# Kernel optimization log

Measured on AMD Instinct MI355X. Metric: run time of the kernel, lower is better.

The kernel has to match this reference:

```python
import jax, jax.numpy as jnp
import numpy as np

N_NODES = 100000
N_EDGES = 1600000
N_GRAPHS = 512
IN_DIM = 128
HID = 128
N_CLASSES = 10


def _gcn_conv(x, W, b, src, dst, n):
    """PyG GCNConv: out = D^{-1/2} (A+I) D^{-1/2} (x @ W) + b."""
    xw = x @ W  # [n, out_dim]
    loop = jnp.arange(n)
    s = jnp.concatenate([src, loop])  # add self loops
    d = jnp.concatenate([dst, loop])
    deg = jax.ops.segment_sum(jnp.ones(s.shape, dtype=xw.dtype), d, num_segments=n)
    dinv = jnp.where(deg > 0, jax.lax.rsqrt(deg), jnp.zeros((), xw.dtype))
    norm = dinv[s] * dinv[d]  # [E + n]
    out = jax.ops.segment_sum(xw[s] * norm[:, None], d, num_segments=n)
    return out + b


def _global_mean_pool(x, batch, num_graphs):
    sums = jax.ops.segment_sum(x, batch, num_segments=num_graphs)
    cnts = jax.ops.segment_sum(jnp.ones(batch.shape, dtype=x.dtype), batch, num_segments=num_graphs)
    return sums / jnp.maximum(cnts, 1.0)[:, None]


def setup_inputs() -> dict:
    key = jax.random.key(0)
    ks = jax.random.split(key, 8)
    x = jax.random.normal(ks[0], (N_NODES, IN_DIM), dtype=jnp.float32)
    edge_index = jax.random.randint(ks[1], (2, N_EDGES), 0, N_NODES, dtype=jnp.int64)
    batch = jnp.sort(jax.random.randint(ks[2], (N_NODES,), 0, N_GRAPHS, dtype=jnp.int64))
    sc = 1.0 / np.sqrt(IN_DIM)
    W1 = jax.random.normal(ks[3], (IN_DIM, HID), dtype=jnp.float32) * sc
    b1 = jnp.zeros((HID,), dtype=jnp.float32)
    W2 = jax.random.normal(ks[4], (HID, HID), dtype=jnp.float32) * (1.0 / np.sqrt(HID))
    b2 = jnp.zeros((HID,), dtype=jnp.float32)
    Wc = jax.random.normal(ks[5], (HID, N_CLASSES), dtype=jnp.float32) * (1.0 / np.sqrt(HID))
    bc = jnp.zeros((N_CLASSES,), dtype=jnp.float32)
    return {"x": x, "edge_index": edge_index, "batch": batch,
            "W1": W1, "b1": b1, "W2": W2, "b2": b2, "Wc": Wc, "bc": bc}


def reference(x, edge_index, batch, W1, b1, W2, b2, Wc, bc):
    src, dst = edge_index[0], edge_index[1]
    n = x.shape[0]
    h = _gcn_conv(x, W1, b1, src, dst, n)
    h = jax.nn.relu(h)
    h = _gcn_conv(h, W2, b2, src, dst, n)
    g = _global_mean_pool(h, batch, N_GRAPHS)
    return g @ Wc + bc
```

## Files before the change

### kernel.cpp

```cpp
#include <hip/hip_runtime.h>

#define N_NODES 100000
#define N_EDGES 1600000
#define N_GRAPHS 512
#define DIM 128
#define NCLS 10
#define NBKT 782
#define BCAP 2560

typedef __attribute__((ext_vector_type(8))) short short8;
typedef __attribute__((ext_vector_type(4))) float f32x4;

static __device__ __forceinline__ unsigned short f2bf(float f) {
    unsigned u = __float_as_uint(f);
    unsigned r = (u + 0x7FFF + ((u >> 16) & 1)) >> 16;
    return (unsigned short)r;
}
static __device__ __forceinline__ float bf2f(unsigned u) {
    return __uint_as_float(u << 16);
}


__global__ void k_zero(int* __restrict__ bcnt) {
    int i = blockIdx.x * 256 + threadIdx.x;
    if (i < NBKT) bcnt[i] = 0;
}

__global__ __launch_bounds__(256) void k_bucket(
    const int* __restrict__ src, const int* __restrict__ dst,
    int* __restrict__ bcnt, unsigned* __restrict__ bpack, int E) {
    __shared__ int cnt[NBKT];
    __shared__ int base[NBKT];
    int tid = threadIdx.x;
    for (int i = tid; i < NBKT; i += 256) cnt[i] = 0;
    __syncthreads();
    int e0 = blockIdx.x * 4096 + tid;
    unsigned pk[16]; short bk[16];
#pragma unroll
    for (int j = 0; j < 16; j++) {
        int e = e0 + j * 256;
        if (e < E) {
            int s = src[e], d = dst[e];
            bk[j] = (short)(d >> 7);
            pk[j] = ((unsigned)(d & 127) << 17) | (unsigned)s;
            atomicAdd(&cnt[bk[j]], 1);
        } else bk[j] = -1;
    }
    __syncthreads();
    for (int i = tid; i < NBKT; i += 256) {
        int c = cnt[i];
        base[i] = c ? atomicAdd(&bcnt[i], c) : 0;
        cnt[i] = 0;
    }
    __syncthreads();
#pragma unroll
    for (int j = 0; j < 16; j++) {
        if (bk[j] >= 0) {
            int p = base[bk[j]] + atomicAdd(&cnt[bk[j]], 1);
            if (p < BCAP) bpack[(size_t)bk[j] * BCAP + p] = pk[j];
        }
    }
}

__global__ __launch_bounds__(256) void k_bscan(const int* __restrict__ bcnt,
                                               int* __restrict__ bbase) {
    __shared__ int lds[256];
    int tid = threadIdx.x;
    int v[4], pre[4];
    int s = 0;
#pragma unroll
    for (int j = 0; j < 4; j++) {
        int idx = tid * 4 + j;
        v[j] = (idx < NBKT) ? min(bcnt[idx], BCAP) : 0;
        pre[j] = s; s += v[j];
    }
    lds[tid] = s;
    __syncthreads();
    for (int off = 1; off < 256; off <<= 1) {
        int t = (tid >= off) ? lds[tid - off] : 0;
        __syncthreads();
        lds[tid] += t;
        __syncthreads();
    }
    int excl = lds[tid] - s;
#pragma unroll
    for (int j = 0; j < 4; j++) {
        int idx = tid * 4 + j;
        if (idx < NBKT) bbase[idx] = excl + pre[j];
    }
}

__global__ __launch_bounds__(256) void k_bsort(
    const unsigned* __restrict__ bpack, const int* __restrict__ bcnt,
    const int* __restrict__ bbase, int* __restrict__ rp, float* __restrict__ dinv,
    int* __restrict__ esrc, int N) {
    __shared__ int cnt[128];
    __shared__ int scan[128];
    __shared__ int cur[128];
    int b = blockIdx.x, tid = threadIdx.x;
    int n0 = b << 7;
    int m = min(bcnt[b], BCAP);
    int gbase = bbase[b];
    const unsigned* bp = bpack + (size_t)b * BCAP;
    if (tid < 128) cnt[tid] = 0;
    __syncthreads();
    for (int j = tid; j < m; j += 256) atomicAdd(&cnt[bp[j] >> 17], 1);
    __syncthreads();
    if (tid < 128) scan[tid] = cnt[tid];
    __syncthreads();
    for (int off = 1; off < 128; off <<= 1) {
        int t = (tid < 128 && tid >= off) ? scan[tid - off] : 0;
        __syncthreads();
        if (tid < 128) scan[tid] += t;
        __syncthreads();
    }
    if (tid < 128) {
        int c = cnt[tid];
        int excl = scan[tid] - c;
        int node = n0 + tid;
        if (node <= N) rp[node] = gbase + excl;
        if (node < N) dinv[node] = rsqrtf((float)(c + 1));
        cur[tid] = gbase + excl;
    }
    __syncthreads();
    for (int j = tid; j < m; j += 256) {
        unsigned pk = bp[j];
        int p = atomicAdd(&cur[pk >> 17], 1);
        esrc[p] = (int)(pk & 0x1FFFF);
    }
}


__global__ void k_wprep(const float* __restrict__ W, unsigned short* __restrict__ wfrag) {
    int t = blockIdx.x * 256 + threadIdx.x;
    int j = t & 7, lane = (t >> 3) & 63, nt = (t >> 9) & 7, kit = t >> 12;
    int k = kit * 32 + (lane >> 4) * 8 + j;
    int n = nt * 16 + (lane & 15);
    float v = W[k * 128 + n];
    unsigned short h = f2bf(v);
    wfrag[t] = h;
    wfrag[16384 + t] = f2bf(v - bf2f(h));
}


__global__ __launch_bounds__(256) void k_gemm_f32(
    const float* __restrict__ A, const unsigned short* __restrict__ wfrag,
    const float* __restrict__ dinv, unsigned short* __restrict__ ybf, int M) {
    __shared__ unsigned short scr[4 * 32 * 136];
    int tid = threadIdx.x, wave = tid >> 6, lane = tid & 63;
    int m = lane & 15, quad = lane >> 4;
    int rowBase = blockIdx.x * 128 + wave * 32;
    int r0 = rowBase + m, r1 = rowBase + 16 + m;
    f32x4 acc0[8], acc1[8];
#pragma unroll
    for (int i = 0; i < 8; i++) { acc0[i] = (f32x4){0,0,0,0}; acc1[i] = (f32x4){0,0,0,0}; }
    const unsigned short* whi = wfrag;
    const unsigned short* wlo = wfrag + 16384;

#pragma unroll
    for (int kit = 0; kit < 4; kit++) {
        float a0[8], a1[8];
        if (r0 < M) {
            const float4* ap = (const float4*)(A + (size_t)r0 * 128 + kit * 32 + quad * 8);
            float4 f0 = ap[0], f1 = ap[1];
            a0[0]=f0.x; a0[1]=f0.y; a0[2]=f0.z; a0[3]=f0.w; a0[4]=f1.x; a0[5]=f1.y; a0[6]=f1.z; a0[7]=f1.w;
        } else { for (int j = 0; j < 8; j++) a0[j] = 0.f; }
        if (r1 < M) {
            const float4* ap = (const float4*)(A + (size_t)r1 * 128 + kit * 32 + quad * 8);
            float4 f0 = ap[0], f1 = ap[1];
            a1[0]=f0.x; a1[1]=f0.y; a1[2]=f0.z; a1[3]=f0.w; a1[4]=f1.x; a1[5]=f1.y; a1[6]=f1.z; a1[7]=f1.w;
        } else { for (int j = 0; j < 8; j++) a1[j] = 0.f; }
        short8 ahi0, alo0, ahi1, alo1;
#pragma unroll
        for (int j = 0; j < 8; j++) {
            unsigned short h0 = f2bf(a0[j]);
            ahi0[j] = (short)h0; alo0[j] = (short)f2bf(a0[j] - bf2f(h0));
            unsigned short h1 = f2bf(a1[j]);
            ahi1[j] = (short)h1; alo1[j] = (short)f2bf(a1[j] - bf2f(h1));
        }
        int fb = kit * 4096 + lane * 8;
#pragma unroll
        for (int nt = 0; nt < 8; nt++) {
            int idx = fb + nt * 512;
            short8 bhi = *(const short8*)(whi + idx);
            short8 blo = *(const short8*)(wlo + idx);
            acc0[nt] = __builtin_amdgcn_mfma_f32_16x16x32_bf16(ahi0, bhi, acc0[nt], 0, 0, 0);
            acc0[nt] = __builtin_amdgcn_mfma_f32_16x16x32_bf16(alo0, bhi, acc0[nt], 0, 0, 0);
            acc0[nt] = __builtin_amdgcn_mfma_f32_16x16x32_bf16(ahi0, blo, acc0[nt], 0, 0, 0);
            acc1[nt] = __builtin_amdgcn_mfma_f32_16x16x32_bf16(ahi1, bhi, acc1[nt], 0, 0, 0);
            acc1[nt] = __builtin_amdgcn_mfma_f32_16x16x32_bf16(alo1, bhi, acc1[nt], 0, 0, 0);
            acc1[nt] = __builtin_amdgcn_mfma_f32_16x16x32_bf16(ahi1, blo, acc1[nt], 0, 0, 0);
        }
    }
    float dv0 = (r0 < M) ? dinv[r0] : 0.f;
    float dv1 = (r1 < M) ? dinv[r1] : 0.f;
    unsigned short* wsm = scr + wave * 32 * 136;
#pragma unroll
    for (int rg = 0; rg < 4; rg++) {
        float s0 = __shfl(dv0, quad * 4 + rg);
        float s1 = __shfl(dv1, quad * 4 + rg);
#pragma unroll
        for (int nt = 0; nt < 8; nt++) {
            wsm[(quad * 4 + rg) * 136 + nt * 16 + m] = f2bf(acc0[nt][rg] * s0);
            wsm[(16 + quad * 4 + rg) * 136 + nt * 16 + m] = f2bf(acc1[nt][rg] * s1);
        }
    }
    __syncthreads();
#pragma unroll
    for (int i = 0; i < 8; i++) {
        int rl = i * 4 + quad;
        int grow = rowBase + rl;
        if (grow < M) {
            short8 v = *(const short8*)(wsm + rl * 136 + m * 8);
            *(short8*)(ybf + (size_t)grow * 128 + m * 8) = v;
        }
    }
}


__global__ __launch_bounds__(256) void k_gemm_bf(
    const unsigned short* __restrict__ A, const unsigned short* __restrict__ wfrag,
    const float* __restrict__ dinv, unsigned short* __restrict__ ybf, int M) {
    __shared__ unsigned short scr[4 * 32 * 136];
    int tid = threadIdx.x, wave = tid >> 6, lane = tid & 63;
    int m = lane & 15, quad = lane >> 4;
    int rowBase = blockIdx.x * 128 + wave * 32;
    int r0 = rowBase + m, r1 = rowBase + 16 + m;
    f32x4 acc0[8], acc1[8];
#pragma unroll
    for (int i = 0; i < 8; i++) { acc0[i] = (f32x4){0,0,0,0}; acc1[i] = (f32x4){0,0,0,0}; }
    const unsigned short* whi = wfrag;
    const unsigned short* wlo = wfrag + 16384;

#pragma unroll
    for (int kit = 0; kit < 4; kit++) {
        short8 ah0, ah1;
        if (r0 < M) ah0 = *(const short8*)(A + (size_t)r0 * 128 + kit * 32 + quad * 8);
        else { for (int j = 0; j < 8; j++) ah0[j] = 0; }
        if (r1 < M) ah1 = *(const short8*)(A + (size_t)r1 * 128 + kit * 32 + quad * 8);
        else { for (int j = 0; j < 8; j++) ah1[j] = 0; }
        int fb = kit * 4096 + lane * 8;
#pragma unroll
        for (int nt = 0; nt < 8; nt++) {
            int idx = fb + nt * 512;
            short8 bhi = *(const short8*)(whi + idx);
            short8 blo = *(const short8*)(wlo + idx);
            acc0[nt] = __builtin_amdgcn_mfma_f32_16x16x32_bf16(ah0, bhi, acc0[nt], 0, 0, 0);
            acc0[nt] = __builtin_amdgcn_mfma_f32_16x16x32_bf16(ah0, blo, acc0[nt], 0, 0, 0);
            acc1[nt] = __builtin_amdgcn_mfma_f32_16x16x32_bf16(ah1, bhi, acc1[nt], 0, 0, 0);
            acc1[nt] = __builtin_amdgcn_mfma_f32_16x16x32_bf16(ah1, blo, acc1[nt], 0, 0, 0);
        }
    }
    float dv0 = (r0 < M) ? dinv[r0] : 0.f;
    float dv1 = (r1 < M) ? dinv[r1] : 0.f;
    unsigned short* wsm = scr + wave * 32 * 136;
#pragma unroll
    for (int rg = 0; rg < 4; rg++) {
        float s0 = __shfl(dv0, quad * 4 + rg);
        float s1 = __shfl(dv1, quad * 4 + rg);
#pragma unroll
        for (int nt = 0; nt < 8; nt++) {
            wsm[(quad * 4 + rg) * 136 + nt * 16 + m] = f2bf(acc0[nt][rg] * s0);
            wsm[(16 + quad * 4 + rg) * 136 + nt * 16 + m] = f2bf(acc1[nt][rg] * s1);
        }
    }
    __syncthreads();
#pragma unroll
    for (int i = 0; i < 8; i++) {
        int rl = i * 4 + quad;
        int grow = rowBase + rl;
        if (grow < M) {
            short8 v = *(const short8*)(wsm + rl * 136 + m * 8);
            *(short8*)(ybf + (size_t)grow * 128 + m * 8) = v;
        }
    }
}


__global__ __launch_bounds__(256) void k_agg(
    const unsigned short* __restrict__ y, const float* __restrict__ dinv,
    const int* __restrict__ rp, const int* __restrict__ esrc,
    const float* __restrict__ bias, unsigned* __restrict__ out, int relu, int N) {
    int wave = threadIdx.x >> 6;
    int lane = threadIdx.x & 63;
    int node = blockIdx.x * 4 + wave;
    if (node >= N) return;
    const unsigned* y2 = (const unsigned*)y;
    unsigned vs = y2[(size_t)node * 64 + lane];
    float a0 = bf2f(vs & 0xFFFF), a1 = bf2f(vs >> 16);
    int beg = rp[node], end = rp[node + 1];
    int j = beg;
    for (; j + 8 <= end; j += 8) {
        int s0 = esrc[j], s1 = esrc[j + 1], s2 = esrc[j + 2], s3 = esrc[j + 3];
        int s4 = esrc[j + 4], s5 = esrc[j + 5], s6 = esrc[j + 6], s7 = esrc[j + 7];
        unsigned v0 = y2[(size_t)s0 * 64 + lane];
        unsigned v1 = y2[(size_t)s1 * 64 + lane];
        unsigned v2 = y2[(size_t)s2 * 64 + lane];
        unsigned v3 = y2[(size_t)s3 * 64 + lane];
        unsigned v4 = y2[(size_t)s4 * 64 + lane];
        unsigned v5 = y2[(size_t)s5 * 64 + lane];
        unsigned v6 = y2[(size_t)s6 * 64 + lane];
        unsigned v7 = y2[(size_t)s7 * 64 + lane];
        a0 += bf2f(v0 & 0xFFFF); a1 += bf2f(v0 >> 16);
        a0 += bf2f(v1 & 0xFFFF); a1 += bf2f(v1 >> 16);
        a0 += bf2f(v2 & 0xFFFF); a1 += bf2f(v2 >> 16);
        a0 += bf2f(v3 & 0xFFFF); a1 += bf2f(v3 >> 16);
        a0 += bf2f(v4 & 0xFFFF); a1 += bf2f(v4 >> 16);
        a0 += bf2f(v5 & 0xFFFF); a1 += bf2f(v5 >> 16);
        a0 += bf2f(v6 & 0xFFFF); a1 += bf2f(v6 >> 16);
        a0 += bf2f(v7 & 0xFFFF); a1 += bf2f(v7 >> 16);
    }
    for (; j < end; j++) {
        unsigned v = y2[(size_t)esrc[j] * 64 + lane];
        a0 += bf2f(v & 0xFFFF); a1 += bf2f(v >> 16);
    }
    float s = dinv[node];
    float2 bv = ((const float2*)bias)[lane];
    float o0 = s * a0 + bv.x;
    float o1 = s * a1 + bv.y;
    if (relu) { o0 = fmaxf(o0, 0.f); o1 = fmaxf(o1, 0.f); }
    out[(size_t)node * 64 + lane] = (unsigned)f2bf(o0) | ((unsigned)f2bf(o1) << 16);
}


__global__ __launch_bounds__(256) void k_pool(
    const unsigned* __restrict__ h2, const int* __restrict__ batch,
    float* __restrict__ g, int n) {
    __shared__ float2 red[4][64];
    int gid = blockIdx.x;
    int tid = threadIdx.x, wave = tid >> 6, lane = tid & 63;
    int lo = 0, hi = n;
    while (lo < hi) { int mid = (lo + hi) >> 1; if (batch[mid] < gid) lo = mid + 1; else hi = mid; }
    int start = lo;
    hi = n;
    while (lo < hi) { int mid = (lo + hi) >> 1; if (batch[mid] < gid + 1) lo = mid + 1; else hi = mid; }
    int end = lo;
    float a0 = 0.f, a1 = 0.f;
    for (int r = start + wave; r < end; r += 4) {
        unsigned v = h2[(size_t)r * 64 + lane];
        a0 += bf2f(v & 0xFFFF); a1 += bf2f(v >> 16);
    }
    red[wave][lane] = make_float2(a0, a1);
    __syncthreads();
    if (tid < 64) {
        float2 s = red[0][tid];
        s.x += red[1][tid].x; s.y += red[1][tid].y;
        s.x += red[2][tid].x; s.y += red[2][tid].y;
        s.x += red[3][tid].x; s.y += red[3][tid].y;
        int cnt = end - start;
        float inv = 1.f / (float)(cnt > 0 ? cnt : 1);
        ((float2*)g)[gid * 64 + tid] = make_float2(s.x * inv, s.y * inv);
    }
}


__global__ __launch_bounds__(128) void k_final(
    const float* __restrict__ g, const float* __restrict__ Wc,
    const float* __restrict__ bc, float* __restrict__ out) {
    __shared__ float row[DIM];
    int gid = blockIdx.x;
    row[threadIdx.x] = g[gid * DIM + threadIdx.x];
    __syncthreads();
    int c = threadIdx.x;
    if (c < NCLS) {
        float acc = bc[c];
#pragma unroll 16
        for (int k = 0; k < DIM; k++) acc += row[k] * Wc[k * NCLS + c];
        out[gid * NCLS + c] = acc;
    }
}

extern "C" void kernel_launch(void* const* d_in, const int* in_sizes, int n_in,
                              void* d_out, int out_size, void* d_ws, size_t ws_size,
                              hipStream_t stream) {
    const float* x    = (const float*)d_in[0];
    const int*   ei   = (const int*)d_in[1];
    const int*   batch= (const int*)d_in[2];
    const float* W1   = (const float*)d_in[3];
    const float* b1   = (const float*)d_in[4];
    const float* W2   = (const float*)d_in[5];
    const float* b2   = (const float*)d_in[6];
    const float* Wc   = (const float*)d_in[7];
    const float* bc   = (const float*)d_in[8];
    float* out = (float*)d_out;
    const int N = N_NODES, E = N_EDGES;
    const int* src = ei;
    const int* dst = ei + E;

    char* ws = (char*)d_ws;
    size_t off = 0;
    auto carve = [&](size_t bytes) -> void* {
        void* p = ws + off;
        off = (off + bytes + 255) & ~(size_t)255;
        return p;
    };
    int*      rp    = (int*)     carve((size_t)(N + 1) * 4);
    float*    dinv  = (float*)   carve((size_t)N * 4);
    int*      bcnt  = (int*)     carve(NBKT * 4);
    int*      bbase = (int*)     carve(NBKT * 4);
    unsigned* bpack = (unsigned*)carve((size_t)NBKT * BCAP * 4);
    int*      esrc  = (int*)     carve((size_t)E * 4);
    unsigned short* wf1 = (unsigned short*)carve(2 * 16384 * 2);
    unsigned short* wf2 = (unsigned short*)carve(2 * 16384 * 2);
    unsigned short* bufY = (unsigned short*)carve((size_t)N * DIM * 2);
    unsigned short* bufH = (unsigned short*)carve((size_t)N * DIM * 2);
    float*    g     = (float*)   carve((size_t)N_GRAPHS * DIM * 4);
    (void)ws_size; (void)n_in; (void)in_sizes; (void)out_size;

    hipLaunchKernelGGL(k_zero,   dim3((NBKT + 255) / 256), dim3(256), 0, stream, bcnt);
    hipLaunchKernelGGL(k_wprep,  dim3(64), dim3(256), 0, stream, W1, wf1);
    hipLaunchKernelGGL(k_wprep,  dim3(64), dim3(256), 0, stream, W2, wf2);
    hipLaunchKernelGGL(k_bucket, dim3((E + 4095) / 4096), dim3(256), 0, stream, src, dst, bcnt, bpack, E);
    hipLaunchKernelGGL(k_bscan,  dim3(1), dim3(256), 0, stream, bcnt, bbase);
    hipLaunchKernelGGL(k_bsort,  dim3(NBKT), dim3(256), 0, stream, bpack, bcnt, bbase, rp, dinv, esrc, N);

    int gemmGrid = (N + 127) / 128;
    hipLaunchKernelGGL(k_gemm_f32, dim3(gemmGrid), dim3(256), 0, stream, x, wf1, dinv, bufY, N);
    hipLaunchKernelGGL(k_agg, dim3((N + 3) / 4), dim3(256), 0, stream, bufY, dinv, rp, esrc, b1, (unsigned*)bufH, 1, N);
    hipLaunchKernelGGL(k_gemm_bf, dim3(gemmGrid), dim3(256), 0, stream, bufH, wf2, dinv, bufY, N);
    hipLaunchKernelGGL(k_agg, dim3((N + 3) / 4), dim3(256), 0, stream, bufY, dinv, rp, esrc, b2, (unsigned*)bufH, 0, N);
    hipLaunchKernelGGL(k_pool,  dim3(N_GRAPHS), dim3(256), 0, stream, (const unsigned*)bufH, batch, g, N);
    hipLaunchKernelGGL(k_final, dim3(N_GRAPHS), dim3(128), 0, stream, g, Wc, bc, out);
}
```

Measured before the change: 377.3 us.

## Store node features in four column-chunk planes for cache-friendly aggregation

The node-feature buffers are split into four planes of 32 bf16 columns each ([4][N][32]). The GEMM epilogues write this layout, the second GEMM reads its A operand from it, and k_agg and k_pool index into it. Aggregation now runs one grid pass per plane with 16 nodes per block, so each gather touches a 64-byte segment and the working set per plane is a quarter of the full table, which should improve L2/MALL hit rates on the random edge gathers. The trade-offs are that edge indices are re-read four times, each gather is a smaller transaction, and the unroll drops from 8 to 4.

```diff
diff --git a/kernel.cpp b/kernel.cpp
--- a/kernel.cpp
+++ b/kernel.cpp
@@ -7,6 +7,7 @@
 #define NCLS 10
 #define NBKT 782
 #define BCAP 2560
+#define BPC 6250
 
 typedef __attribute__((ext_vector_type(8))) short short8;
 typedef __attribute__((ext_vector_type(4))) float f32x4;
@@ -212,7 +213,7 @@
         int grow = rowBase + rl;
         if (grow < M) {
             short8 v = *(const short8*)(wsm + rl * 136 + m * 8);
-            *(short8*)(ybf + (size_t)grow * 128 + m * 8) = v;
+            *(short8*)(ybf + ((size_t)(m >> 2) * M + grow) * 32 + (m & 3) * 8) = v;
         }
     }
 }
@@ -235,9 +236,9 @@
 #pragma unroll
     for (int kit = 0; kit < 4; kit++) {
         short8 ah0, ah1;
-        if (r0 < M) ah0 = *(const short8*)(A + (size_t)r0 * 128 + kit * 32 + quad * 8);
+        if (r0 < M) ah0 = *(const short8*)(A + ((size_t)kit * M + r0) * 32 + quad * 8);
         else { for (int j = 0; j < 8; j++) ah0[j] = 0; }
-        if (r1 < M) ah1 = *(const short8*)(A + (size_t)r1 * 128 + kit * 32 + quad * 8);
+        if (r1 < M) ah1 = *(const short8*)(A + ((size_t)kit * M + r1) * 32 + quad * 8);
         else { for (int j = 0; j < 8; j++) ah1[j] = 0; }
         int fb = kit * 4096 + lane * 8;
 #pragma unroll
@@ -271,55 +272,47 @@
         int grow = rowBase + rl;
         if (grow < M) {
             short8 v = *(const short8*)(wsm + rl * 136 + m * 8);
-            *(short8*)(ybf + (size_t)grow * 128 + m * 8) = v;
+            *(short8*)(ybf + ((size_t)(m >> 2) * M + grow) * 32 + (m & 3) * 8) = v;
         }
     }
 }
 
 
 __global__ __launch_bounds__(256) void k_agg(
-    const unsigned short* __restrict__ y, const float* __restrict__ dinv,
+    const unsigned* __restrict__ y2, const float* __restrict__ dinv,
     const int* __restrict__ rp, const int* __restrict__ esrc,
     const float* __restrict__ bias, unsigned* __restrict__ out, int relu, int N) {
-    int wave = threadIdx.x >> 6;
-    int lane = threadIdx.x & 63;
-    int node = blockIdx.x * 4 + wave;
-    if (node >= N) return;
-    const unsigned* y2 = (const unsigned*)y;
-    unsigned vs = y2[(size_t)node * 64 + lane];
+    int c = blockIdx.x / BPC;
+    int nb = blockIdx.x - c * BPC;
+    int node = nb * 16 + (threadIdx.x >> 4);
+    int i = threadIdx.x & 15;
+    const unsigned* yc = y2 + (size_t)c * N * 16;
+    unsigned vs = yc[(size_t)node * 16 + i];
     float a0 = bf2f(vs & 0xFFFF), a1 = bf2f(vs >> 16);
     int beg = rp[node], end = rp[node + 1];
     int j = beg;
-    for (; j + 8 <= end; j += 8) {
+    for (; j + 4 <= end; j += 4) {
         int s0 = esrc[j], s1 = esrc[j + 1], s2 = esrc[j + 2], s3 = esrc[j + 3];
-        int s4 = esrc[j + 4], s5 = esrc[j + 5], s6 = esrc[j + 6], s7 = esrc[j + 7];
-        unsigned v0 = y2[(size_t)s0 * 64 + lane];
-        unsigned v1 = y2[(size_t)s1 * 64 + lane];
-        unsigned v2 = y2[(size_t)s2 * 64 + lane];
-        unsigned v3 = y2[(size_t)s3 * 64 + lane];
-        unsigned v4 = y2[(size_t)s4 * 64 + lane];
-        unsigned v5 = y2[(size_t)s5 * 64 + lane];
-        unsigned v6 = y2[(size_t)s6 * 64 + lane];
-        unsigned v7 = y2[(size_t)s7 * 64 + lane];
+        unsigned v0 = yc[(size_t)s0 * 16 + i];
+        unsigned v1 = yc[(size_t)s1 * 16 + i];
+        unsigned v2 = yc[(size_t)s2 * 16 + i];
+        unsigned v3 = yc[(size_t)s3 * 16 + i];
         a0 += bf2f(v0 & 0xFFFF); a1 += bf2f(v0 >> 16);
         a0 += bf2f(v1 & 0xFFFF); a1 += bf2f(v1 >> 16);
         a0 += bf2f(v2 & 0xFFFF); a1 += bf2f(v2 >> 16);
         a0 += bf2f(v3 & 0xFFFF); a1 += bf2f(v3 >> 16);
-        a0 += bf2f(v4 & 0xFFFF); a1 += bf2f(v4 >> 16);
-        a0 += bf2f(v5 & 0xFFFF); a1 += bf2f(v5 >> 16);
-        a0 += bf2f(v6 & 0xFFFF); a1 += bf2f(v6 >> 16);
-        a0 += bf2f(v7 & 0xFFFF); a1 += bf2f(v7 >> 16);
     }
     for (; j < end; j++) {
-        unsigned v = y2[(size_t)esrc[j] * 64 + lane];
+        unsigned v = yc[(size_t)esrc[j] * 16 + i];
         a0 += bf2f(v & 0xFFFF); a1 += bf2f(v >> 16);
     }
     float s = dinv[node];
-    float2 bv = ((const float2*)bias)[lane];
+    float2 bv = ((const float2*)bias)[c * 16 + i];
     float o0 = s * a0 + bv.x;
     float o1 = s * a1 + bv.y;
     if (relu) { o0 = fmaxf(o0, 0.f); o1 = fmaxf(o1, 0.f); }
-    out[(size_t)node * 64 + lane] = (unsigned)f2bf(o0) | ((unsigned)f2bf(o1) << 16);
+    out[(size_t)c * N * 16 + (size_t)node * 16 + i] =
+        (unsigned)f2bf(o0) | ((unsigned)f2bf(o1) << 16);
 }
 
 
@@ -328,19 +321,20 @@
     float* __restrict__ g, int n) {
     __shared__ float2 red[4][64];
     int gid = blockIdx.x;
-    int tid = threadIdx.x, wave = tid >> 6, lane = tid & 63;
+    int tid = threadIdx.x, wave = tid >> 6, p = tid & 63;
     int lo = 0, hi = n;
     while (lo < hi) { int mid = (lo + hi) >> 1; if (batch[mid] < gid) lo = mid + 1; else hi = mid; }
     int start = lo;
     hi = n;
     while (lo < hi) { int mid = (lo + hi) >> 1; if (batch[mid] < gid + 1) lo = mid + 1; else hi = mid; }
     int end = lo;
+    const unsigned* hc = h2 + (size_t)(p >> 4) * n * 16;
     float a0 = 0.f, a1 = 0.f;
     for (int r = start + wave; r < end; r += 4) {
-        unsigned v = h2[(size_t)r * 64 + lane];
+        unsigned v = hc[(size_t)r * 16 + (p & 15)];
         a0 += bf2f(v & 0xFFFF); a1 += bf2f(v >> 16);
     }
-    red[wave][lane] = make_float2(a0, a1);
+    red[wave][p] = make_float2(a0, a1);
     __syncthreads();
     if (tid < 64) {
         float2 s = red[0][tid];
@@ -415,10 +409,11 @@
     hipLaunchKernelGGL(k_bsort,  dim3(NBKT), dim3(256), 0, stream, bpack, bcnt, bbase, rp, dinv, esrc, N);
 
     int gemmGrid = (N + 127) / 128;
+    int aggGrid = 4 * BPC;
     hipLaunchKernelGGL(k_gemm_f32, dim3(gemmGrid), dim3(256), 0, stream, x, wf1, dinv, bufY, N);
-    hipLaunchKernelGGL(k_agg, dim3((N + 3) / 4), dim3(256), 0, stream, bufY, dinv, rp, esrc, b1, (unsigned*)bufH, 1, N);
+    hipLaunchKernelGGL(k_agg, dim3(aggGrid), dim3(256), 0, stream, (const unsigned*)bufY, dinv, rp, esrc, b1, (unsigned*)bufH, 1, N);
     hipLaunchKernelGGL(k_gemm_bf, dim3(gemmGrid), dim3(256), 0, stream, bufH, wf2, dinv, bufY, N);
-    hipLaunchKernelGGL(k_agg, dim3((N + 3) / 4), dim3(256), 0, stream, bufY, dinv, rp, esrc, b2, (unsigned*)bufH, 0, N);
+    hipLaunchKernelGGL(k_agg, dim3(aggGrid), dim3(256), 0, stream, (const unsigned*)bufY, dinv, rp, esrc, b2, (unsigned*)bufH, 0, N);
     hipLaunchKernelGGL(k_pool,  dim3(N_GRAPHS), dim3(256), 0, stream, (const unsigned*)bufH, batch, g, N);
     hipLaunchKernelGGL(k_final, dim3(N_GRAPHS), dim3(128), 0, stream, g, Wc, bc, out);
 }
```

After: 405.9 us. 7.6% more time.
